# Performance work log

Hardware: AMD Instinct MI355X
Metric: run time of the kernel (lower is better)

Reference implementation:

```python
import jax, jax.numpy as jnp
import numpy as np

N_LAYERS = 2
D_MODEL = 1024
D_INNER = 2048  # expand=2
D_STATE = 16
D_CONV = 4
DT_RANK = 64    # ceil(d_model/16)
N_CLASSES = 10
B, L = 4, 1024


def setup_inputs() -> dict:
    key = jax.random.key(0)
    ks = jax.random.split(key, 20)
    s = 0.02
    inp = {
        'x': jax.random.normal(ks[0], (B, L, D_MODEL), jnp.float32),
        'ln1_w': jnp.ones((N_LAYERS, D_MODEL), jnp.float32),
        'ln1_b': jnp.zeros((N_LAYERS, D_MODEL), jnp.float32),
        'in_proj_w': jax.random.normal(ks[1], (N_LAYERS, 2 * D_INNER, D_MODEL), jnp.float32) * s,
        'conv_w': jax.random.normal(ks[2], (N_LAYERS, D_INNER, D_CONV), jnp.float32) * 0.2,
        'conv_b': jnp.zeros((N_LAYERS, D_INNER), jnp.float32),
        'x_proj_w': jax.random.normal(ks[3], (N_LAYERS, DT_RANK + 2 * D_STATE, D_INNER), jnp.float32) * s,
        'dt_proj_w': jax.random.normal(ks[4], (N_LAYERS, D_INNER, DT_RANK), jnp.float32) * 0.1,
        'dt_proj_b': jax.random.normal(ks[5], (N_LAYERS, D_INNER), jnp.float32) * 0.1 - 4.6,  # softplus -> dt ~ 0.01
        'A_log': jnp.broadcast_to(jnp.log(jnp.arange(1, D_STATE + 1, dtype=jnp.float32)), (N_LAYERS, D_INNER, D_STATE)) + 0.0,
        'D_param': jnp.ones((N_LAYERS, D_INNER), jnp.float32),
        'out_proj_w': jax.random.normal(ks[6], (N_LAYERS, D_MODEL, D_INNER), jnp.float32) * s,
        'norm_w': jnp.ones((D_MODEL,), jnp.float32),
        'norm_b': jnp.zeros((D_MODEL,), jnp.float32),
        'head_w': jax.random.normal(ks[7], (N_CLASSES, D_MODEL), jnp.float32) * s,
        'head_b': jnp.zeros((N_CLASSES,), jnp.float32),
    }
    return inp


def _layernorm(x, w, b, eps=1e-5):
    mu = jnp.mean(x, axis=-1, keepdims=True)
    var = jnp.var(x, axis=-1, keepdims=True)
    return (x - mu) * jax.lax.rsqrt(var + eps) * w + b


def _selective_scan(xc, dt, A, Bm, Cm, D):
    # xc, dt: (B, L, D_INNER); Bm, Cm: (B, L, D_STATE); A: (D_INNER, D_STATE); D: (D_INNER,)
    def step(h, inp):
        dt_t, B_t, C_t, xc_t = inp  # (B,C),(B,N),(B,N),(B,C)
        dA = jnp.exp(dt_t[..., None] * A)            # (B, C, N)
        h = dA * h + (dt_t * xc_t)[..., None] * B_t[:, None, :]
        y = jnp.einsum('bcn,bn->bc', h, C_t)
        return h, y

    h0 = jnp.zeros((xc.shape[0], A.shape[0], A.shape[1]), xc.dtype)
    xs = (dt.transpose(1, 0, 2), Bm.transpose(1, 0, 2), Cm.transpose(1, 0, 2), xc.transpose(1, 0, 2))
    _, ys = jax.lax.scan(step, h0, xs)
    y = ys.transpose(1, 0, 2)  # (B, L, C)
    return y + xc * D


def _mamba_layer(x, ln_w, ln_b, in_w, cw, cb, xp_w, dtp_w, dtp_b, A_log, D, out_w):
    h = _layernorm(x, ln_w, ln_b)
    xz = jnp.einsum('bld,ed->ble', h, in_w)          # (B, L, 2*D_INNER)
    x_in, z = jnp.split(xz, 2, axis=-1)
    # causal depthwise conv1d, kernel D_CONV
    xp = jnp.pad(x_in, ((0, 0), (D_CONV - 1, 0), (0, 0)))
    conv = cb
    for k in range(D_CONV):
        conv = conv + cw[:, k] * xp[:, k:k + x_in.shape[1], :]
    xc = jax.nn.silu(conv)
    x_dbl = jnp.einsum('blc,ec->ble', xc, xp_w)
    dt_r = x_dbl[..., :DT_RANK]
    Bm = x_dbl[..., DT_RANK:DT_RANK + D_STATE]
    Cm = x_dbl[..., DT_RANK + D_STATE:]
    dt = jax.nn.softplus(jnp.einsum('blr,cr->blc', dt_r, dtp_w) + dtp_b)
    A = -jnp.exp(A_log)
    y = _selective_scan(xc, dt, A, Bm, Cm, D)
    y = y * jax.nn.silu(z)
    return x + jnp.einsum('blc,dc->bld', y, out_w)


def reference(x, ln1_w, ln1_b, in_proj_w, conv_w, conv_b, x_proj_w, dt_proj_w, dt_proj_b,
              A_log, D_param, out_proj_w, norm_w, norm_b, head_w, head_b):
    for i in range(N_LAYERS):
        x = _mamba_layer(x, ln1_w[i], ln1_b[i], in_proj_w[i], conv_w[i], conv_b[i],
                         x_proj_w[i], dt_proj_w[i], dt_proj_b[i], A_log[i], D_param[i], out_proj_w[i])
    x = _layernorm(x, norm_w, norm_b)
    pooled = jnp.mean(x, axis=1)  # (B, D_MODEL)
    return pooled @ head_w.T + head_b
```

## Files before the change

### kernel.cpp

```cpp
#include <hip/hip_runtime.h>
#include <hip/hip_bf16.h>

#define N_LAYERS 2
#define D_MODEL 1024
#define D_INNER 2048
#define D_STATE 16
#define D_CONV 4
#define DT_RANK 64
#define N_CLASSES 10
#define BB 4
#define LL 1024
#define BL (BB*LL)
#define CH 32
#define CLEN (LL/CH)
#define KS 8
#define KSO 2

typedef __attribute__((ext_vector_type(8))) short bf16x8;
typedef __attribute__((ext_vector_type(8))) unsigned short us8;
typedef __attribute__((ext_vector_type(4))) float f32x4;

typedef const void __attribute__((address_space(1)))* gas_ptr;
typedef void __attribute__((address_space(3)))* las_ptr;
#define GLDS16(g, p) __builtin_amdgcn_global_load_lds((gas_ptr)(g), (las_ptr)(p), 16, 0, 0)

__device__ inline unsigned short rnd_bf16(float x) {
  unsigned u = __float_as_uint(x);
  return (unsigned short)((u + 0x7FFFu + ((u >> 16) & 1u)) >> 16);
}
__device__ inline float b2f(unsigned short u) {
  return __uint_as_float(((unsigned)u) << 16);
}

__global__ __launch_bounds__(256) void round_k(const float* __restrict__ in,
    unsigned short* __restrict__ hi) {
  const int i = blockIdx.x * 256 + threadIdx.x;
  const float4 v = ((const float4*)in)[i];
  ushort4 h4;
  h4.x = rnd_bf16(v.x); h4.y = rnd_bf16(v.y);
  h4.z = rnd_bf16(v.z); h4.w = rnd_bf16(v.w);
  ((ushort4*)hi)[i] = h4;
}

__global__ __launch_bounds__(256) void layernorm_bf16_k(const float* __restrict__ x,
    const float* __restrict__ w, const float* __restrict__ b,
    unsigned short* __restrict__ oh) {
  const int row = blockIdx.x;
  const int t = threadIdx.x;
  const float4 v = *(const float4*)(x + (size_t)row * D_MODEL + t * 4);
  float s = v.x + v.y + v.z + v.w;
  float q = v.x*v.x + v.y*v.y + v.z*v.z + v.w*v.w;
  #pragma unroll
  for (int o = 32; o; o >>= 1) { s += __shfl_down(s, o); q += __shfl_down(q, o); }
  __shared__ float red[8];
  if ((t & 63) == 0) { red[t >> 6] = s; red[4 + (t >> 6)] = q; }
  __syncthreads();
  s = red[0] + red[1] + red[2] + red[3];
  q = red[4] + red[5] + red[6] + red[7];
  const float mean = s * (1.f / D_MODEL);
  const float var  = q * (1.f / D_MODEL) - mean * mean;
  const float rstd = rsqrtf(var + 1e-5f);
  const float4 wv = *(const float4*)(w + t * 4);
  const float4 bv = *(const float4*)(b + t * 4);
  ushort4 h4;
  h4.x = rnd_bf16((v.x - mean) * rstd * wv.x + bv.x);
  h4.y = rnd_bf16((v.y - mean) * rstd * wv.y + bv.y);
  h4.z = rnd_bf16((v.z - mean) * rstd * wv.z + bv.z);
  h4.w = rnd_bf16((v.w - mean) * rstd * wv.w + bv.w);
  ((ushort4*)(oh + (size_t)row * D_MODEL))[t] = h4;
}

template<int OUT>
__global__ __launch_bounds__(256) void oreduce_ln_k(
    const float* __restrict__ part, const float* __restrict__ Xin,
    float* __restrict__ Xout,
    const float* __restrict__ w, const float* __restrict__ b,
    void* __restrict__ out) {
  const int row = blockIdx.x;
  const int t = threadIdx.x;
  float4 v = *(const float4*)(Xin + (size_t)row * D_MODEL + t * 4);
  #pragma unroll
  for (int k = 0; k < KSO; k++) {
    const float4 p = *(const float4*)(part + (size_t)k * BL * D_MODEL
                                      + (size_t)row * D_MODEL + t * 4);
    v.x += p.x; v.y += p.y; v.z += p.z; v.w += p.w;
  }
  *(float4*)(Xout + (size_t)row * D_MODEL + t * 4) = v;
  float s = v.x + v.y + v.z + v.w;
  float q = v.x*v.x + v.y*v.y + v.z*v.z + v.w*v.w;
  #pragma unroll
  for (int o = 32; o; o >>= 1) { s += __shfl_down(s, o); q += __shfl_down(q, o); }
  __shared__ float red[8];
  if ((t & 63) == 0) { red[t >> 6] = s; red[4 + (t >> 6)] = q; }
  __syncthreads();
  s = red[0] + red[1] + red[2] + red[3];
  q = red[4] + red[5] + red[6] + red[7];
  const float mean = s * (1.f / D_MODEL);
  const float var  = q * (1.f / D_MODEL) - mean * mean;
  const float rstd = rsqrtf(var + 1e-5f);
  const float4 wv = *(const float4*)(w + t * 4);
  const float4 bv = *(const float4*)(b + t * 4);
  float4 o4;
  o4.x = (v.x - mean) * rstd * wv.x + bv.x;
  o4.y = (v.y - mean) * rstd * wv.y + bv.y;
  o4.z = (v.z - mean) * rstd * wv.z + bv.z;
  o4.w = (v.w - mean) * rstd * wv.w + bv.w;
  if constexpr (OUT == 0) {
    ushort4 h4;
    h4.x = rnd_bf16(o4.x); h4.y = rnd_bf16(o4.y);
    h4.z = rnd_bf16(o4.z); h4.w = rnd_bf16(o4.w);
    ((ushort4*)((unsigned short*)out + (size_t)row * D_MODEL))[t] = h4;
  } else {
    *(float4*)((float*)out + (size_t)row * D_MODEL + t * 4) = o4;
  }
}

__global__ __launch_bounds__(512) void mfma_gemm256_nt(
    const unsigned short* __restrict__ A, const unsigned short* __restrict__ B,
    unsigned short* __restrict__ C, int K, int ldc) {
  __shared__ unsigned short S[65536];
  const int tid = threadIdx.x;
  const int l = tid & 63;
  const int w = tid >> 6;
  const int wm = w >> 2, wn = w & 3;
  const int bid = blockIdx.y * 16 + blockIdx.x;
  const int x = bid & 7, v = bid >> 3;
  const int bx = (x & 1) * 8 + (v & 7);
  const int by = (x >> 1) * 4 + (v >> 3);
  const int m0 = by * 256, n0 = bx * 256;
  const int nkt = K >> 6;
  const int r8 = (tid >> 3) & 7;
  const int c16s = (tid & 7) ^ r8;

  auto stage1 = [&](int kt, int mat, int half) {
    const unsigned short* base = (mat == 0) ? (A + (size_t)m0 * K)
                                            : (B + (size_t)n0 * K);
    unsigned short* dst = S + ((kt & 1) * 32768 + mat * 16384 + half * 8192);
    #pragma unroll
    for (int e = 0; e < 2; ++e) {
      const int row = half * 128 + e * 64 + (tid >> 3);
      GLDS16(base + (size_t)row * K + kt * 64 + c16s * 8,
             dst + e * 4096 + tid * 8);
    }
  };
  auto stage_full = [&](int kt) {
    stage1(kt, 0, 0); stage1(kt, 0, 1); stage1(kt, 1, 0); stage1(kt, 1, 1);
  };

  stage_full(0);
  if (nkt > 1) stage_full(1);

  f32x4 acc[8][4] = {};
  const int fr = l & 15;
  const int fk8 = l >> 4;

  #pragma unroll 1
  for (int kt = 0; kt < nkt; ++kt) {
    if (kt + 1 < nkt) asm volatile("s_waitcnt vmcnt(8)" ::: "memory");
    else              asm volatile("s_waitcnt vmcnt(0)" ::: "memory");
    __builtin_amdgcn_s_barrier();
    __builtin_amdgcn_sched_barrier(0);
    const unsigned short* SA = S + (kt & 1) * 32768;
    const unsigned short* SB = SA + 16384;
    #pragma unroll
    for (int kk8 = 0; kk8 < 8; kk8 += 4) {
      bf16x8 av[8], bv[4];
      const int c8 = kk8 + fk8;
      #pragma unroll
      for (int i = 0; i < 8; ++i) {
        const int R = wm * 128 + i * 16 + fr;
        av[i] = *(const bf16x8*)&SA[R * 64 + ((c8 ^ (R & 7)) << 3)];
      }
      #pragma unroll
      for (int j = 0; j < 4; ++j) {
        const int R = wn * 64 + j * 16 + fr;
        bv[j] = *(const bf16x8*)&SB[R * 64 + ((c8 ^ (R & 7)) << 3)];
      }
      __builtin_amdgcn_s_setprio(1);
      #pragma unroll
      for (int i = 0; i < 8; ++i)
        #pragma unroll
        for (int j = 0; j < 4; ++j)
          acc[i][j] = __builtin_amdgcn_mfma_f32_16x16x32_bf16(
              av[i], bv[j], acc[i][j], 0, 0, 0);
      __builtin_amdgcn_s_setprio(0);
    }
    __builtin_amdgcn_s_barrier();
    __builtin_amdgcn_sched_barrier(0);
    if (kt + 2 < nkt) stage_full(kt + 2);
  }

  const int orow = (l >> 4) * 4, ocol = l & 15;
  #pragma unroll
  for (int i = 0; i < 8; ++i)
    #pragma unroll
    for (int j = 0; j < 4; ++j)
      #pragma unroll
      for (int r = 0; r < 4; ++r) {
        const int m = m0 + wm * 128 + i * 16 + orow + r;
        const int n = n0 + wn * 64 + j * 16 + ocol;
        C[(size_t)m * ldc + n] = rnd_bf16(acc[i][j][r]);
      }
}

template<int EPI, int KSEG>
__global__ __launch_bounds__(256) void mfma_gemm_nt(
    const unsigned short* __restrict__ Ah, const unsigned short* __restrict__ Bh,
    void* __restrict__ Cv, int M, int N, int K, int ldc) {
  __shared__ unsigned short As[128 * 64];
  __shared__ unsigned short Bs[128 * 64];
  const int tid = threadIdx.x;
  const int w = tid >> 6, l = tid & 63;
  const int wr = w >> 1, wc = w & 1;
  const int nbx = gridDim.x;
  const int nwg = nbx * gridDim.y;
  int bid = blockIdx.y * nbx + blockIdx.x;
  bid = (bid & 7) * (nwg >> 3) + (bid >> 3);
  const int st = bid >> 6, wi = bid & 63;
  const int stpr = (nbx >= 8) ? (nbx >> 3) : 1;
  int n0, m0;
  if (nbx >= 8) {
    n0 = ((st % stpr) * 8 + (wi & 7)) * 128;
    m0 = ((st / stpr) * 8 + (wi >> 3)) * 128;
  } else {
    n0 = (bid % nbx) * 128;
    m0 = (bid / nbx) * 128;
  }
  const int kz = (KSEG > 1) ? blockIdx.z : 0;
  const int kbeg = kz * (K / KSEG);
  const int kend = kbeg + K / KSEG;
  const int srow = l >> 3;
  const int scol = (l & 7) * 8;
  const int fr = l & 15;
  const int fk = (l >> 4) * 8;
  f32x4 acc[4][4] = {};

  #pragma unroll 1
  for (int k0 = kbeg; k0 < kend; k0 += 64) {
    __syncthreads();
    #pragma unroll
    for (int it = 0; it < 4; ++it) {
      const int bi = it * 4 + w;
      const int row = bi * 8 + srow;
      GLDS16(Ah + (size_t)(m0 + row) * K + k0 + scol, &As[bi * 512 + l * 8]);
      GLDS16(Bh + (size_t)(n0 + row) * K + k0 + scol, &Bs[bi * 512 + l * 8]);
    }
    __syncthreads();
    #pragma unroll
    for (int kk = 0; kk < 64; kk += 32) {
      bf16x8 a[4], b[4];
      #pragma unroll
      for (int f = 0; f < 4; ++f)
        b[f] = *(const bf16x8*)&Bs[(wc * 64 + f * 16 + fr) * 64 + kk + fk];
      #pragma unroll
      for (int f = 0; f < 4; ++f)
        a[f] = *(const bf16x8*)&As[(wr * 64 + f * 16 + fr) * 64 + kk + fk];
      #pragma unroll
      for (int i = 0; i < 4; ++i)
        #pragma unroll
        for (int j = 0; j < 4; ++j)
          acc[i][j] = __builtin_amdgcn_mfma_f32_16x16x32_bf16(
              a[i], b[j], acc[i][j], 0, 0, 0);
    }
  }
  const int orow = (l >> 4) * 4;
  const int ocol = l & 15;
  if constexpr (EPI == 0) {
    unsigned short* Cw = (unsigned short*)Cv;
    #pragma unroll
    for (int i = 0; i < 4; ++i)
      #pragma unroll
      for (int j = 0; j < 4; ++j)
        #pragma unroll
        for (int r = 0; r < 4; ++r) {
          const int m = m0 + wr * 64 + i * 16 + orow + r;
          const int n = n0 + wc * 64 + j * 16 + ocol;
          Cw[(size_t)m * ldc + n] = rnd_bf16(acc[i][j][r]);
        }
  } else {
    float* Cw = (float*)Cv + (size_t)kz * M * ldc;
    #pragma unroll
    for (int i = 0; i < 4; ++i)
      #pragma unroll
      for (int j = 0; j < 4; ++j)
        #pragma unroll
        for (int r = 0; r < 4; ++r) {
          const int m = m0 + wr * 64 + i * 16 + orow + r;
          const int n = n0 + wc * 64 + j * 16 + ocol;
          Cw[(size_t)m * ldc + n] = acc[i][j][r];
        }
  }
}

template<int BM, int BN, int BK, int TM, int TN, int EPI>
__global__ __launch_bounds__(256) void sgemm_nt(
    const float* __restrict__ A, const float* __restrict__ B,
    void* __restrict__ Cv, int M, int N, int K, int lda, int ldb, int ldc,
    const float* __restrict__ bias) {
  constexpr int THREADS = 256;
  constexpr int NT = BN / TN;
  constexpr int K4 = BK / 4;
  constexpr int A_F4 = BM * BK / (THREADS * 4);
  constexpr int B_F4 = BN * BK / (THREADS * 4);
  static_assert((BM / TM) * (BN / TN) == THREADS, "thread shape");
  __shared__ float As[BK][BM + 4];
  __shared__ float Bs[BK][BN + 4];
  const int tid = threadIdx.x;
  const int m0 = blockIdx.y * BM;
  const int n0 = blockIdx.x * BN;
  const int tn = (tid % NT) * TN;
  const int tm = (tid / NT) * TM;
  float acc[TM][TN] = {};
  for (int k0 = 0; k0 < K; k0 += BK) {
    #pragma unroll
    for (int i = 0; i < A_F4; i++) {
      int li = tid + i * THREADS;
      int r = li / K4, c4 = li % K4;
      float4 v = *(const float4*)(A + (size_t)(m0 + r) * lda + k0 + c4 * 4);
      As[c4*4+0][r] = v.x; As[c4*4+1][r] = v.y; As[c4*4+2][r] = v.z; As[c4*4+3][r] = v.w;
    }
    #pragma unroll
    for (int i = 0; i < B_F4; i++) {
      int li = tid + i * THREADS;
      int r = li / K4, c4 = li % K4;
      float4 v = *(const float4*)(B + (size_t)(n0 + r) * ldb + k0 + c4 * 4);
      Bs[c4*4+0][r] = v.x; Bs[c4*4+1][r] = v.y; Bs[c4*4+2][r] = v.z; Bs[c4*4+3][r] = v.w;
    }
    __syncthreads();
    #pragma unroll
    for (int k = 0; k < BK; k++) {
      float a[TM], bf[TN];
      #pragma unroll
      for (int i = 0; i < TM; i++) a[i] = As[k][tm + i];
      #pragma unroll
      for (int j = 0; j < TN; j++) bf[j] = Bs[k][tn + j];
      #pragma unroll
      for (int i = 0; i < TM; i++)
        #pragma unroll
        for (int j = 0; j < TN; j++)
          acc[i][j] = fmaf(a[i], bf[j], acc[i][j]);
    }
    __syncthreads();
  }
  #pragma unroll
  for (int i = 0; i < TM; i++) {
    const int m = m0 + tm + i;
    #pragma unroll
    for (int j = 0; j < TN; j++) {
      const int n = n0 + tn + j;
      float v = acc[i][j];
      if constexpr (EPI == 1) {
        v += bias[n];
        v = (v > 20.f) ? v : log1pf(__expf(v));
        ((unsigned short*)Cv)[(size_t)m * ldc + n] = rnd_bf16(v);
      } else {
        ((float*)Cv)[(size_t)m * ldc + n] = v;
      }
    }
  }
}

__global__ __launch_bounds__(256) void sgemm_splitk_k(
    const unsigned short* __restrict__ A, const float* __restrict__ B,
    float* __restrict__ part) {
  __shared__ float As[32][64 + 4];
  __shared__ float Bs[32][32 + 4];
  const int tid = threadIdx.x;
  const int n0 = blockIdx.x * 32;
  const int m0 = blockIdx.y * 64;
  const int kz = blockIdx.z;
  const int tn = (tid & 15) * 2;
  const int tm = (tid >> 4) * 4;
  float acc[4][2] = {};
  for (int kb = 0; kb < 256; kb += 32) {
    const int k0 = kz * 256 + kb;
    {
      int r = tid >> 2, c8 = (tid & 3) * 8;
      us8 u = *(const us8*)(A + (size_t)(m0 + r) * D_INNER + k0 + c8);
      #pragma unroll
      for (int j = 0; j < 8; j++) As[c8 + j][r] = b2f((unsigned short)u[j]);
    }
    {
      int r = tid >> 3, c4 = tid & 7;
      float4 v = *(const float4*)(B + (size_t)(n0 + r) * D_INNER + k0 + c4 * 4);
      Bs[c4*4+0][r] = v.x; Bs[c4*4+1][r] = v.y;
      Bs[c4*4+2][r] = v.z; Bs[c4*4+3][r] = v.w;
    }
    __syncthreads();
    #pragma unroll
    for (int k = 0; k < 32; k++) {
      float a[4], bf[2];
      #pragma unroll
      for (int i = 0; i < 4; i++) a[i] = As[k][tm + i];
      bf[0] = Bs[k][tn]; bf[1] = Bs[k][tn + 1];
      #pragma unroll
      for (int i = 0; i < 4; i++) {
        acc[i][0] = fmaf(a[i], bf[0], acc[i][0]);
        acc[i][1] = fmaf(a[i], bf[1], acc[i][1]);
      }
    }
    __syncthreads();
  }
  float* p = part + (size_t)kz * BL * 96;
  #pragma unroll
  for (int i = 0; i < 4; i++) {
    const int m = m0 + tm + i;
    p[(size_t)m * 96 + n0 + tn]     = acc[i][0];
    p[(size_t)m * 96 + n0 + tn + 1] = acc[i][1];
  }
}

__global__ __launch_bounds__(256) void xproj_reduce_k(
    const float* __restrict__ part, float* __restrict__ out) {
  const int i = blockIdx.x * 256 + threadIdx.x;
  float s = 0.f;
  #pragma unroll
  for (int k = 0; k < KS; k++) s += part[(size_t)k * BL * 96 + i];
  out[i] = s;
}

__global__ __launch_bounds__(256) void conv_silu_k(
    const unsigned short* __restrict__ xz,
    const float* __restrict__ cw, const float* __restrict__ cb,
    unsigned short* __restrict__ xc) {
  const int gid = blockIdx.x * 256 + threadIdx.x;
  const int c4 = (gid & (D_INNER / 4 - 1)) << 2;
  const int row = gid >> 9;
  const int l = row & (LL - 1);
  const unsigned short* base = xz + (size_t)row * (2 * D_INNER) + c4;
  const float4 w0 = *(const float4*)(cw + (c4 + 0) * 4);
  const float4 w1 = *(const float4*)(cw + (c4 + 1) * 4);
  const float4 w2 = *(const float4*)(cw + (c4 + 2) * 4);
  const float4 w3 = *(const float4*)(cw + (c4 + 3) * 4);
  float4 acc = *(const float4*)(cb + c4);
  ushort4 uv = *(const ushort4*)base;
  acc.x = fmaf(w0.w, b2f(uv.x), acc.x); acc.y = fmaf(w1.w, b2f(uv.y), acc.y);
  acc.z = fmaf(w2.w, b2f(uv.z), acc.z); acc.w = fmaf(w3.w, b2f(uv.w), acc.w);
  if (l >= 1) {
    uv = *(const ushort4*)(base - 2 * D_INNER);
    acc.x = fmaf(w0.z, b2f(uv.x), acc.x); acc.y = fmaf(w1.z, b2f(uv.y), acc.y);
    acc.z = fmaf(w2.z, b2f(uv.z), acc.z); acc.w = fmaf(w3.z, b2f(uv.w), acc.w);
  }
  if (l >= 2) {
    uv = *(const ushort4*)(base - 4 * D_INNER);
    acc.x = fmaf(w0.y, b2f(uv.x), acc.x); acc.y = fmaf(w1.y, b2f(uv.y), acc.y);
    acc.z = fmaf(w2.y, b2f(uv.z), acc.z); acc.w = fmaf(w3.y, b2f(uv.w), acc.w);
  }
  if (l >= 3) {
    uv = *(const ushort4*)(base - 6 * D_INNER);
    acc.x = fmaf(w0.x, b2f(uv.x), acc.x); acc.y = fmaf(w1.x, b2f(uv.y), acc.y);
    acc.z = fmaf(w2.x, b2f(uv.z), acc.z); acc.w = fmaf(w3.x, b2f(uv.w), acc.w);
  }
  ushort4 o4;
  o4.x = rnd_bf16(acc.x / (1.f + __expf(-acc.x)));
  o4.y = rnd_bf16(acc.y / (1.f + __expf(-acc.y)));
  o4.z = rnd_bf16(acc.z / (1.f + __expf(-acc.z)));
  o4.w = rnd_bf16(acc.w / (1.f + __expf(-acc.w)));
  *(ushort4*)(xc + (size_t)row * D_INNER + c4) = o4;
}

__global__ __launch_bounds__(256) void scan_pass1_k(
    const unsigned short* __restrict__ dt, const unsigned short* __restrict__ xc,
    const float* __restrict__ xdbl, const float* __restrict__ A_log,
    float* __restrict__ hend, float* __restrict__ sumdt) {
  const int c = blockIdx.x * 256 + threadIdx.x;
  const int k = blockIdx.y;
  const int b = blockIdx.z;
  float Ac[D_STATE];
  #pragma unroll
  for (int n = 0; n < D_STATE; n++) Ac[n] = -__expf(A_log[c * D_STATE + n]);
  float h[D_STATE] = {};
  float sd = 0.f;
  const size_t r0 = (size_t)b * LL + (size_t)k * CLEN;
  const unsigned short* dtp = dt + r0 * D_INNER + c;
  const unsigned short* xcp = xc + r0 * D_INNER + c;
  const float* Bp  = xdbl + r0 * 96 + DT_RANK;

  float dtv = b2f(dtp[0]);
  float xv  = b2f(xcp[0]);
  float4 B0 = *(const float4*)(Bp + 0);
  float4 B1 = *(const float4*)(Bp + 4);
  float4 B2 = *(const float4*)(Bp + 8);
  float4 B3 = *(const float4*)(Bp + 12);
  for (int l = 0; l < CLEN; l++) {
    const int lp = (l + 1 < CLEN) ? l + 1 : l;
    const float dtv2 = b2f(dtp[(size_t)lp * D_INNER]);
    const float xv2  = b2f(xcp[(size_t)lp * D_INNER]);
    const float4 B0n = *(const float4*)(Bp + (size_t)lp * 96 + 0);
    const float4 B1n = *(const float4*)(Bp + (size_t)lp * 96 + 4);
    const float4 B2n = *(const float4*)(Bp + (size_t)lp * 96 + 8);
    const float4 B3n = *(const float4*)(Bp + (size_t)lp * 96 + 12);
    sd += dtv;
    const float dx = dtv * xv;
    const float Bv[D_STATE] = {B0.x,B0.y,B0.z,B0.w, B1.x,B1.y,B1.z,B1.w,
                               B2.x,B2.y,B2.z,B2.w, B3.x,B3.y,B3.z,B3.w};
    #pragma unroll
    for (int n = 0; n < D_STATE; n++)
      h[n] = fmaf(__expf(dtv * Ac[n]), h[n], dx * Bv[n]);
    dtv = dtv2; xv = xv2; B0 = B0n; B1 = B1n; B2 = B2n; B3 = B3n;
  }
  float* he = hend + (((size_t)(b * CH + k) * D_INNER + c) << 4);
  #pragma unroll
  for (int n = 0; n < D_STATE; n += 4)
    *(float4*)(he + n) = make_float4(h[n], h[n+1], h[n+2], h[n+3]);
  sumdt[(size_t)(b * CH + k) * D_INNER + c] = sd;
}

__global__ __launch_bounds__(256) void scan_fix_k(
    float* __restrict__ hend, const float* __restrict__ sumdt,
    const float* __restrict__ A_log) {
  const int gid = blockIdx.x * 256 + threadIdx.x;
  const int n = gid & 15;
  const int c = (gid >> 4) & (D_INNER - 1);
  const int b = gid >> 15;
  const float Ac = -__expf(A_log[c * D_STATE + n]);
  float hrun = 0.f;
  for (int k = 0; k < CH; k++) {
    const size_t base = (size_t)(b * CH + k) * D_INNER + c;
    const float sd = sumdt[base];
    float* hp = hend + (base << 4) + n;
    const float tmp = *hp;
    *hp = hrun;
    hrun = fmaf(__expf(Ac * sd), hrun, tmp);
  }
}

__global__ __launch_bounds__(256) void scan_pass3_k(
    const unsigned short* __restrict__ dt, const unsigned short* __restrict__ xc,
    const float* __restrict__ xdbl, const unsigned short* __restrict__ xz,
    const float* __restrict__ h0, const float* __restrict__ A_log,
    const float* __restrict__ Dp, unsigned short* __restrict__ yh) {
  const int c = blockIdx.x * 256 + threadIdx.x;
  const int k = blockIdx.y;
  const int b = blockIdx.z;
  float Ac[D_STATE];
  #pragma unroll
  for (int n = 0; n < D_STATE; n++) Ac[n] = -__expf(A_log[c * D_STATE + n]);
  const float Dv = Dp[c];
  float h[D_STATE];
  const float* hp = h0 + (((size_t)(b * CH + k) * D_INNER + c) << 4);
  #pragma unroll
  for (int n = 0; n < D_STATE; n += 4) {
    const float4 v = *(const float4*)(hp + n);
    h[n] = v.x; h[n+1] = v.y; h[n+2] = v.z; h[n+3] = v.w;
  }
  const size_t r0 = (size_t)b * LL + (size_t)k * CLEN;
  const unsigned short* dtp = dt + r0 * D_INNER + c;
  const unsigned short* xcp = xc + r0 * D_INNER + c;
  const float* Bp  = xdbl + r0 * 96 + DT_RANK;
  const unsigned short* zp = xz + r0 * (size_t)(2 * D_INNER) + D_INNER + c;
  unsigned short* yhp = yh + r0 * D_INNER + c;

  float dtv = b2f(dtp[0]);
  float xv  = b2f(xcp[0]);
  float zv  = b2f(zp[0]);
  float4 B0 = *(const float4*)(Bp + 0);
  float4 B1 = *(const float4*)(Bp + 4);
  float4 B2 = *(const float4*)(Bp + 8);
  float4 B3 = *(const float4*)(Bp + 12);
  float4 C0 = *(const float4*)(Bp + 16);
  float4 C1 = *(const float4*)(Bp + 20);
  float4 C2 = *(const float4*)(Bp + 24);
  float4 C3 = *(const float4*)(Bp + 28);
  for (int l = 0; l < CLEN; l++) {
    const int lp = (l + 1 < CLEN) ? l + 1 : l;
    const float dtv2 = b2f(dtp[(size_t)lp * D_INNER]);
    const float xv2  = b2f(xcp[(size_t)lp * D_INNER]);
    const float zv2  = b2f(zp[(size_t)lp * 2 * D_INNER]);
    const float4 B0n = *(const float4*)(Bp + (size_t)lp * 96 + 0);
    const float4 B1n = *(const float4*)(Bp + (size_t)lp * 96 + 4);
    const float4 B2n = *(const float4*)(Bp + (size_t)lp * 96 + 8);
    const float4 B3n = *(const float4*)(Bp + (size_t)lp * 96 + 12);
    const float4 C0n = *(const float4*)(Bp + (size_t)lp * 96 + 16);
    const float4 C1n = *(const float4*)(Bp + (size_t)lp * 96 + 20);
    const float4 C2n = *(const float4*)(Bp + (size_t)lp * 96 + 24);
    const float4 C3n = *(const float4*)(Bp + (size_t)lp * 96 + 28);
    const float dx = dtv * xv;
    const float Bv[D_STATE] = {B0.x,B0.y,B0.z,B0.w, B1.x,B1.y,B1.z,B1.w,
                               B2.x,B2.y,B2.z,B2.w, B3.x,B3.y,B3.z,B3.w};
    const float Cv[D_STATE] = {C0.x,C0.y,C0.z,C0.w, C1.x,C1.y,C1.z,C1.w,
                               C2.x,C2.y,C2.z,C2.w, C3.x,C3.y,C3.z,C3.w};
    float y = 0.f;
    #pragma unroll
    for (int n = 0; n < D_STATE; n++) {
      h[n] = fmaf(__expf(dtv * Ac[n]), h[n], dx * Bv[n]);
      y = fmaf(h[n], Cv[n], y);
    }
    y = fmaf(xv, Dv, y);
    y *= zv / (1.f + __expf(-zv));
    yhp[(size_t)l * D_INNER] = rnd_bf16(y);
    dtv = dtv2; xv = xv2; zv = zv2;
    B0 = B0n; B1 = B1n; B2 = B2n; B3 = B3n;
    C0 = C0n; C1 = C1n; C2 = C2n; C3 = C3n;
  }
}

__global__ __launch_bounds__(256) void pool1_k(const float* __restrict__ h,
    float* __restrict__ pp) {
  const int d = blockIdx.x * 256 + threadIdx.x;
  const int b = blockIdx.y;
  const int seg = blockIdx.z;
  float s = 0.f;
  const size_t base = (size_t)b * LL + (size_t)seg * 64;
  for (int l = 0; l < 64; l++) s += h[(base + l) * D_MODEL + d];
  pp[((size_t)(b * 16 + seg)) * D_MODEL + d] = s;
}
__global__ __launch_bounds__(256) void pool2_k(const float* __restrict__ pp,
    float* __restrict__ pooled) {
  const int d = blockIdx.x * 256 + threadIdx.x;
  const int b = blockIdx.y;
  float s = 0.f;
  #pragma unroll
  for (int k = 0; k < 16; k++) s += pp[((size_t)(b * 16 + k)) * D_MODEL + d];
  pooled[b * D_MODEL + d] = s * (1.f / LL);
}

__global__ __launch_bounds__(64) void head_k(const float* __restrict__ pooled,
    const float* __restrict__ hw, const float* __restrict__ hb,
    float* __restrict__ out) {
  const int b = blockIdx.x / N_CLASSES;
  const int j = blockIdx.x % N_CLASSES;
  float s = 0.f;
  for (int k = threadIdx.x; k < D_MODEL; k += 64)
    s = fmaf(pooled[b * D_MODEL + k], hw[j * D_MODEL + k], s);
  #pragma unroll
  for (int o = 32; o; o >>= 1) s += __shfl_down(s, o);
  if (threadIdx.x == 0) out[b * N_CLASSES + j] = s + hb[j];
}

extern "C" void kernel_launch(void* const* d_in, const int* in_sizes, int n_in,
                              void* d_out, int out_size, void* d_ws, size_t ws_size,
                              hipStream_t stream) {
  const float* x0    = (const float*)d_in[0];
  const float* ln1w  = (const float*)d_in[1];
  const float* ln1b  = (const float*)d_in[2];
  const float* inw   = (const float*)d_in[3];
  const float* convw = (const float*)d_in[4];
  const float* convb = (const float*)d_in[5];
  const float* xpw   = (const float*)d_in[6];
  const float* dtpw  = (const float*)d_in[7];
  const float* dtpb  = (const float*)d_in[8];
  const float* Alog  = (const float*)d_in[9];
  const float* Dp    = (const float*)d_in[10];
  const float* outw  = (const float*)d_in[11];
  const float* normw = (const float*)d_in[12];
  const float* normb = (const float*)d_in[13];
  const float* headw = (const float*)d_in[14];
  const float* headb = (const float*)d_in[15];

  float* ws = (float*)d_ws;
  size_t f = 0;
  float* X      = ws + f; f += (size_t)BL * D_MODEL;
  float* xzf    = ws + f; f += (size_t)BL * D_INNER;
  float* xdbl   = ws + f; f += (size_t)BL * 96;
  float* dty    = ws + f; f += (size_t)BL * D_INNER;
  float* pooled = ws + f; f += 4096;
  float* pooldp = ws + f; f += (size_t)16 * BB * D_MODEL;
  float* xpart  = ws + f; f += (size_t)KS * BL * 96;
  float* hend   = ws + f; f += (size_t)BB * CH * D_INNER * D_STATE;
  float* opart  = ws + f; f += (size_t)KSO * BL * D_MODEL;
  unsigned short* hh  = (unsigned short*)(ws + f); f += (size_t)BL * D_MODEL / 2;
  unsigned short* yh  = (unsigned short*)(ws + f); f += (size_t)BL * D_INNER / 2;
  unsigned short* xcb = (unsigned short*)(ws + f); f += (size_t)BL * D_INNER / 2;
  unsigned short* wih = (unsigned short*)(ws + f);
  f += (size_t)N_LAYERS * 2 * D_INNER * D_MODEL / 2;
  unsigned short* woh = (unsigned short*)(ws + f);
  f += (size_t)N_LAYERS * D_MODEL * D_INNER / 2;
  unsigned short* xz  = (unsigned short*)xzf;
  unsigned short* dtb = (unsigned short*)dty;
  float* sumdt = xpart;

  round_k<<<(N_LAYERS * 2 * D_INNER * D_MODEL) / 1024, 256, 0, stream>>>(inw, wih);
  round_k<<<(N_LAYERS * D_MODEL * D_INNER) / 1024, 256, 0, stream>>>(outw, woh);
  layernorm_bf16_k<<<BL, 256, 0, stream>>>(x0, ln1w, ln1b, hh);

  for (int layer = 0; layer < N_LAYERS; ++layer) {
    const unsigned short* wi = wih + (size_t)layer * 2 * D_INNER * D_MODEL;
    const unsigned short* wo = woh + (size_t)layer * D_MODEL * D_INNER;
    mfma_gemm256_nt<<<dim3(16, 16), 512, 0, stream>>>(
        hh, wi, xz, D_MODEL, 2 * D_INNER);
    conv_silu_k<<<(BL * D_INNER / 4) / 256, 256, 0, stream>>>(
        xz, convw + layer * D_INNER * D_CONV, convb + layer * D_INNER, xcb);
    sgemm_splitk_k<<<dim3(96 / 32, 4096 / 64, KS), 256, 0, stream>>>(
        xcb, xpw + (size_t)layer * 96 * D_INNER, xpart);
    xproj_reduce_k<<<(BL * 96) / 256, 256, 0, stream>>>(xpart, xdbl);
    sgemm_nt<64,64,64,4,4,1><<<dim3(2048 / 64, 4096 / 64), 256, 0, stream>>>(
        xdbl, dtpw + (size_t)layer * D_INNER * DT_RANK, dtb,
        BL, D_INNER, DT_RANK, 96, DT_RANK, D_INNER,
        dtpb + layer * D_INNER);
    scan_pass1_k<<<dim3(D_INNER / 256, CH, BB), 256, 0, stream>>>(
        dtb, xcb, xdbl, Alog + (size_t)layer * D_INNER * D_STATE, hend, sumdt);
    scan_fix_k<<<(BB * D_INNER * D_STATE) / 256, 256, 0, stream>>>(
        hend, sumdt, Alog + (size_t)layer * D_INNER * D_STATE);
    scan_pass3_k<<<dim3(D_INNER / 256, CH, BB), 256, 0, stream>>>(
        dtb, xcb, xdbl, xz, hend, Alog + (size_t)layer * D_INNER * D_STATE,
        Dp + layer * D_INNER, yh);
    mfma_gemm_nt<1, KSO><<<dim3(1024 / 128, 4096 / 128, KSO), 256, 0, stream>>>(
        yh, wo, opart, BL, D_MODEL, D_INNER, D_MODEL);
    const float* Xin = (layer == 0) ? x0 : X;
    if (layer + 1 < N_LAYERS) {
      oreduce_ln_k<0><<<BL, 256, 0, stream>>>(
          opart, Xin, X, ln1w + (layer + 1) * D_MODEL,
          ln1b + (layer + 1) * D_MODEL, hh);
    } else {
      oreduce_ln_k<1><<<BL, 256, 0, stream>>>(opart, Xin, X, normw, normb, dty);
    }
  }

  pool1_k<<<dim3(D_MODEL / 256, BB, 16), 256, 0, stream>>>(dty, pooldp);
  pool2_k<<<dim3(D_MODEL / 256, BB), 256, 0, stream>>>(pooldp, pooled);
  head_k<<<BB * N_CLASSES, 64, 0, stream>>>(pooled, headw, headb, (float*)d_out);
}
```

Before: 570.7 us.

## Run dt_proj GEMM on bf16 MFMA with fused softplus epilogue

Replaces the fp32 SIMT sgemm for the dt projection with the existing bf16 MFMA GEMM, adding an epilogue that applies bias and softplus. The x_proj reduction now writes the dt-rank slice as bf16 and packs B/C into a dense 32-wide fp32 buffer, which shrinks the stride of the scan kernels' B/C loads. The dt_proj weights are rounded to bf16 up front. This trades fp32 precision for dt_r and its weights against faster matrix-core throughput, and adds one small weight conversion launch.

```diff
diff --git a/kernel.cpp b/kernel.cpp
--- a/kernel.cpp
+++ b/kernel.cpp
@@ -206,7 +206,8 @@
 template<int EPI, int KSEG>
 __global__ __launch_bounds__(256) void mfma_gemm_nt(
     const unsigned short* __restrict__ Ah, const unsigned short* __restrict__ Bh,
-    void* __restrict__ Cv, int M, int N, int K, int ldc) {
+    void* __restrict__ Cv, int M, int N, int K, int ldc,
+    const float* __restrict__ bias) {
   __shared__ unsigned short As[128 * 64];
   __shared__ unsigned short Bs[128 * 64];
   const int tid = threadIdx.x;
@@ -265,7 +266,7 @@
   }
   const int orow = (l >> 4) * 4;
   const int ocol = l & 15;
-  if constexpr (EPI == 0) {
+  if constexpr (EPI == 0 || EPI == 2) {
     unsigned short* Cw = (unsigned short*)Cv;
     #pragma unroll
     for (int i = 0; i < 4; ++i)
@@ -275,7 +276,12 @@
         for (int r = 0; r < 4; ++r) {
           const int m = m0 + wr * 64 + i * 16 + orow + r;
           const int n = n0 + wc * 64 + j * 16 + ocol;
-          Cw[(size_t)m * ldc + n] = rnd_bf16(acc[i][j][r]);
+          float vv = acc[i][j][r];
+          if constexpr (EPI == 2) {
+            vv += bias[n];
+            vv = (vv > 20.f) ? vv : log1pf(__expf(vv));
+          }
+          Cw[(size_t)m * ldc + n] = rnd_bf16(vv);
         }
   } else {
     float* Cw = (float*)Cv + (size_t)kz * M * ldc;
@@ -289,74 +295,6 @@
           const int n = n0 + wc * 64 + j * 16 + ocol;
           Cw[(size_t)m * ldc + n] = acc[i][j][r];
         }
-  }
-}
-
-template<int BM, int BN, int BK, int TM, int TN, int EPI>
-__global__ __launch_bounds__(256) void sgemm_nt(
-    const float* __restrict__ A, const float* __restrict__ B,
-    void* __restrict__ Cv, int M, int N, int K, int lda, int ldb, int ldc,
-    const float* __restrict__ bias) {
-  constexpr int THREADS = 256;
-  constexpr int NT = BN / TN;
-  constexpr int K4 = BK / 4;
-  constexpr int A_F4 = BM * BK / (THREADS * 4);
-  constexpr int B_F4 = BN * BK / (THREADS * 4);
-  static_assert((BM / TM) * (BN / TN) == THREADS, "thread shape");
-  __shared__ float As[BK][BM + 4];
-  __shared__ float Bs[BK][BN + 4];
-  const int tid = threadIdx.x;
-  const int m0 = blockIdx.y * BM;
-  const int n0 = blockIdx.x * BN;
-  const int tn = (tid % NT) * TN;
-  const int tm = (tid / NT) * TM;
-  float acc[TM][TN] = {};
-  for (int k0 = 0; k0 < K; k0 += BK) {
-    #pragma unroll
-    for (int i = 0; i < A_F4; i++) {
-      int li = tid + i * THREADS;
-      int r = li / K4, c4 = li % K4;
-      float4 v = *(const float4*)(A + (size_t)(m0 + r) * lda + k0 + c4 * 4);
-      As[c4*4+0][r] = v.x; As[c4*4+1][r] = v.y; As[c4*4+2][r] = v.z; As[c4*4+3][r] = v.w;
-    }
-    #pragma unroll
-    for (int i = 0; i < B_F4; i++) {
-      int li = tid + i * THREADS;
-      int r = li / K4, c4 = li % K4;
-      float4 v = *(const float4*)(B + (size_t)(n0 + r) * ldb + k0 + c4 * 4);
-      Bs[c4*4+0][r] = v.x; Bs[c4*4+1][r] = v.y; Bs[c4*4+2][r] = v.z; Bs[c4*4+3][r] = v.w;
-    }
-    __syncthreads();
-    #pragma unroll
-    for (int k = 0; k < BK; k++) {
-      float a[TM], bf[TN];
-      #pragma unroll
-      for (int i = 0; i < TM; i++) a[i] = As[k][tm + i];
-      #pragma unroll
-      for (int j = 0; j < TN; j++) bf[j] = Bs[k][tn + j];
-      #pragma unroll
-      for (int i = 0; i < TM; i++)
-        #pragma unroll
-        for (int j = 0; j < TN; j++)
-          acc[i][j] = fmaf(a[i], bf[j], acc[i][j]);
-    }
-    __syncthreads();
-  }
-  #pragma unroll
-  for (int i = 0; i < TM; i++) {
-    const int m = m0 + tm + i;
-    #pragma unroll
-    for (int j = 0; j < TN; j++) {
-      const int n = n0 + tn + j;
-      float v = acc[i][j];
-      if constexpr (EPI == 1) {
-        v += bias[n];
-        v = (v > 20.f) ? v : log1pf(__expf(v));
-        ((unsigned short*)Cv)[(size_t)m * ldc + n] = rnd_bf16(v);
-      } else {
-        ((float*)Cv)[(size_t)m * ldc + n] = v;
-      }
-    }
   }
 }
 
@@ -411,12 +349,15 @@
 }
 
 __global__ __launch_bounds__(256) void xproj_reduce_k(
-    const float* __restrict__ part, float* __restrict__ out) {
+    const float* __restrict__ part, unsigned short* __restrict__ dtr,
+    float* __restrict__ bc) {
   const int i = blockIdx.x * 256 + threadIdx.x;
+  const int m = i / 96, col = i % 96;
   float s = 0.f;
   #pragma unroll
   for (int k = 0; k < KS; k++) s += part[(size_t)k * BL * 96 + i];
-  out[i] = s;
+  if (col < DT_RANK) dtr[(size_t)m * DT_RANK + col] = rnd_bf16(s);
+  else               bc[(size_t)m * 32 + (col - DT_RANK)] = s;
 }
 
 __global__ __launch_bounds__(256) void conv_silu_k(
@@ -461,7 +402,7 @@
 
 __global__ __launch_bounds__(256) void scan_pass1_k(
     const unsigned short* __restrict__ dt, const unsigned short* __restrict__ xc,
-    const float* __restrict__ xdbl, const float* __restrict__ A_log,
+    const float* __restrict__ bc, const float* __restrict__ A_log,
     float* __restrict__ hend, float* __restrict__ sumdt) {
   const int c = blockIdx.x * 256 + threadIdx.x;
   const int k = blockIdx.y;
@@ -474,7 +415,7 @@
   const size_t r0 = (size_t)b * LL + (size_t)k * CLEN;
   const unsigned short* dtp = dt + r0 * D_INNER + c;
   const unsigned short* xcp = xc + r0 * D_INNER + c;
-  const float* Bp  = xdbl + r0 * 96 + DT_RANK;
+  const float* Bp  = bc + r0 * 32;
 
   float dtv = b2f(dtp[0]);
   float xv  = b2f(xcp[0]);
@@ -486,10 +427,10 @@
     const int lp = (l + 1 < CLEN) ? l + 1 : l;
     const float dtv2 = b2f(dtp[(size_t)lp * D_INNER]);
     const float xv2  = b2f(xcp[(size_t)lp * D_INNER]);
-    const float4 B0n = *(const float4*)(Bp + (size_t)lp * 96 + 0);
-    const float4 B1n = *(const float4*)(Bp + (size_t)lp * 96 + 4);
-    const float4 B2n = *(const float4*)(Bp + (size_t)lp * 96 + 8);
-    const float4 B3n = *(const float4*)(Bp + (size_t)lp * 96 + 12);
+    const float4 B0n = *(const float4*)(Bp + (size_t)lp * 32 + 0);
+    const float4 B1n = *(const float4*)(Bp + (size_t)lp * 32 + 4);
+    const float4 B2n = *(const float4*)(Bp + (size_t)lp * 32 + 8);
+    const float4 B3n = *(const float4*)(Bp + (size_t)lp * 32 + 12);
     sd += dtv;
     const float dx = dtv * xv;
     const float Bv[D_STATE] = {B0.x,B0.y,B0.z,B0.w, B1.x,B1.y,B1.z,B1.w,
@@ -527,7 +468,7 @@
 
 __global__ __launch_bounds__(256) void scan_pass3_k(
     const unsigned short* __restrict__ dt, const unsigned short* __restrict__ xc,
-    const float* __restrict__ xdbl, const unsigned short* __restrict__ xz,
+    const float* __restrict__ bc, const unsigned short* __restrict__ xz,
     const float* __restrict__ h0, const float* __restrict__ A_log,
     const float* __restrict__ Dp, unsigned short* __restrict__ yh) {
   const int c = blockIdx.x * 256 + threadIdx.x;
@@ -547,7 +488,7 @@
   const size_t r0 = (size_t)b * LL + (size_t)k * CLEN;
   const unsigned short* dtp = dt + r0 * D_INNER + c;
   const unsigned short* xcp = xc + r0 * D_INNER + c;
-  const float* Bp  = xdbl + r0 * 96 + DT_RANK;
+  const float* Bp  = bc + r0 * 32;
   const unsigned short* zp = xz + r0 * (size_t)(2 * D_INNER) + D_INNER + c;
   unsigned short* yhp = yh + r0 * D_INNER + c;
 
@@ -567,14 +508,14 @@
     const float dtv2 = b2f(dtp[(size_t)lp * D_INNER]);
     const float xv2  = b2f(xcp[(size_t)lp * D_INNER]);
     const float zv2  = b2f(zp[(size_t)lp * 2 * D_INNER]);
-    const float4 B0n = *(const float4*)(Bp + (size_t)lp * 96 + 0);
-    const float4 B1n = *(const float4*)(Bp + (size_t)lp * 96 + 4);
-    const float4 B2n = *(const float4*)(Bp + (size_t)lp * 96 + 8);
-    const float4 B3n = *(const float4*)(Bp + (size_t)lp * 96 + 12);
-    const float4 C0n = *(const float4*)(Bp + (size_t)lp * 96 + 16);
-    const float4 C1n = *(const float4*)(Bp + (size_t)lp * 96 + 20);
-    const float4 C2n = *(const float4*)(Bp + (size_t)lp * 96 + 24);
-    const float4 C3n = *(const float4*)(Bp + (size_t)lp * 96 + 28);
+    const float4 B0n = *(const float4*)(Bp + (size_t)lp * 32 + 0);
+    const float4 B1n = *(const float4*)(Bp + (size_t)lp * 32 + 4);
+    const float4 B2n = *(const float4*)(Bp + (size_t)lp * 32 + 8);
+    const float4 B3n = *(const float4*)(Bp + (size_t)lp * 32 + 12);
+    const float4 C0n = *(const float4*)(Bp + (size_t)lp * 32 + 16);
+    const float4 C1n = *(const float4*)(Bp + (size_t)lp * 32 + 20);
+    const float4 C2n = *(const float4*)(Bp + (size_t)lp * 32 + 24);
+    const float4 C3n = *(const float4*)(Bp + (size_t)lp * 32 + 28);
     const float dx = dtv * xv;
     const float Bv[D_STATE] = {B0.x,B0.y,B0.z,B0.w, B1.x,B1.y,B1.z,B1.w,
                                B2.x,B2.y,B2.z,B2.w, B3.x,B3.y,B3.z,B3.w};
@@ -652,7 +593,7 @@
   size_t f = 0;
   float* X      = ws + f; f += (size_t)BL * D_MODEL;
   float* xzf    = ws + f; f += (size_t)BL * D_INNER;
-  float* xdbl   = ws + f; f += (size_t)BL * 96;
+  float* bc     = ws + f; f += (size_t)BL * 32;
   float* dty    = ws + f; f += (size_t)BL * D_INNER;
   float* pooled = ws + f; f += 4096;
   float* pooldp = ws + f; f += (size_t)16 * BB * D_MODEL;
@@ -662,41 +603,44 @@
   unsigned short* hh  = (unsigned short*)(ws + f); f += (size_t)BL * D_MODEL / 2;
   unsigned short* yh  = (unsigned short*)(ws + f); f += (size_t)BL * D_INNER / 2;
   unsigned short* xcb = (unsigned short*)(ws + f); f += (size_t)BL * D_INNER / 2;
+  unsigned short* dtr = (unsigned short*)(ws + f); f += (size_t)BL * DT_RANK / 2;
   unsigned short* wih = (unsigned short*)(ws + f);
   f += (size_t)N_LAYERS * 2 * D_INNER * D_MODEL / 2;
   unsigned short* woh = (unsigned short*)(ws + f);
   f += (size_t)N_LAYERS * D_MODEL * D_INNER / 2;
+  unsigned short* wdt = (unsigned short*)(ws + f);
+  f += (size_t)N_LAYERS * D_INNER * DT_RANK / 2;
   unsigned short* xz  = (unsigned short*)xzf;
   unsigned short* dtb = (unsigned short*)dty;
   float* sumdt = xpart;
 
   round_k<<<(N_LAYERS * 2 * D_INNER * D_MODEL) / 1024, 256, 0, stream>>>(inw, wih);
   round_k<<<(N_LAYERS * D_MODEL * D_INNER) / 1024, 256, 0, stream>>>(outw, woh);
+  round_k<<<(N_LAYERS * D_INNER * DT_RANK) / 1024, 256, 0, stream>>>(dtpw, wdt);
   layernorm_bf16_k<<<BL, 256, 0, stream>>>(x0, ln1w, ln1b, hh);
 
   for (int layer = 0; layer < N_LAYERS; ++layer) {
     const unsigned short* wi = wih + (size_t)layer * 2 * D_INNER * D_MODEL;
     const unsigned short* wo = woh + (size_t)layer * D_MODEL * D_INNER;
+    const unsigned short* wd = wdt + (size_t)layer * D_INNER * DT_RANK;
     mfma_gemm256_nt<<<dim3(16, 16), 512, 0, stream>>>(
         hh, wi, xz, D_MODEL, 2 * D_INNER);
     conv_silu_k<<<(BL * D_INNER / 4) / 256, 256, 0, stream>>>(
         xz, convw + layer * D_INNER * D_CONV, convb + layer * D_INNER, xcb);
     sgemm_splitk_k<<<dim3(96 / 32, 4096 / 64, KS), 256, 0, stream>>>(
         xcb, xpw + (size_t)layer * 96 * D_INNER, xpart);
-    xproj_reduce_k<<<(BL * 96) / 256, 256, 0, stream>>>(xpart, xdbl);
-    sgemm_nt<64,64,64,4,4,1><<<dim3(2048 / 64, 4096 / 64), 256, 0, stream>>>(
-        xdbl, dtpw + (size_t)layer * D_INNER * DT_RANK, dtb,
-        BL, D_INNER, DT_RANK, 96, DT_RANK, D_INNER,
-        dtpb + layer * D_INNER);
+    xproj_reduce_k<<<(BL * 96) / 256, 256, 0, stream>>>(xpart, dtr, bc);
+    mfma_gemm_nt<2, 1><<<dim3(2048 / 128, 4096 / 128), 256, 0, stream>>>(
+        dtr, wd, dtb, BL, D_INNER, DT_RANK, D_INNER, dtpb + layer * D_INNER);
     scan_pass1_k<<<dim3(D_INNER / 256, CH, BB), 256, 0, stream>>>(
-        dtb, xcb, xdbl, Alog + (size_t)layer * D_INNER * D_STATE, hend, sumdt);
+        dtb, xcb, bc, Alog + (size_t)layer * D_INNER * D_STATE, hend, sumdt);
     scan_fix_k<<<(BB * D_INNER * D_STATE) / 256, 256, 0, stream>>>(
         hend, sumdt, Alog + (size_t)layer * D_INNER * D_STATE);
     scan_pass3_k<<<dim3(D_INNER / 256, CH, BB), 256, 0, stream>>>(
-        dtb, xcb, xdbl, xz, hend, Alog + (size_t)layer * D_INNER * D_STATE,
+        dtb, xcb, bc, xz, hend, Alog + (size_t)layer * D_INNER * D_STATE,
         Dp + layer * D_INNER, yh);
     mfma_gemm_nt<1, KSO><<<dim3(1024 / 128, 4096 / 128, KSO), 256, 0, stream>>>(
-        yh, wo, opart, BL, D_MODEL, D_INNER, D_MODEL);
+        yh, wo, opart, BL, D_MODEL, D_INNER, D_MODEL, nullptr);
     const float* Xin = (layer == 0) ? x0 : X;
     if (layer + 1 < N_LAYERS) {
       oreduce_ln_k<0><<<BL, 256, 0, stream>>>(
```

Measured after the change: 553.1 us. 1.03x faster.
